# Kernel optimization log

Hardware: AMD Instinct MI355X
Metric: run time of the kernel (lower is better)

## Reference

```python
import jax, jax.numpy as jnp
import numpy as np

N_NODES = 100000
N_EDGES = 3200000
DROP_P = 0.5


def gcn_conv(x, W, b, src, dst, deg_inv_sqrt, n):
    # PyG GCNConv with self-loops already folded into (src, dst):
    # out[j] = sum_{(i->j)} dinv[i]*dinv[j] * (x W)[i] + b
    h = x @ W
    norm = deg_inv_sqrt[src] * deg_inv_sqrt[dst]          # [E+N]
    msg = h[src] * norm[:, None]                          # [E+N, d_out]
    out = jax.ops.segment_sum(msg, dst, num_segments=n)
    return out + b


def dropout(x, key, p=DROP_P):
    keep = jax.random.bernoulli(key, 1.0 - p, x.shape)
    return jnp.where(keep, x / (1.0 - p), 0.0)


def setup_inputs() -> dict:
    key = jax.random.key(0)
    ks = jax.random.split(key, 8)
    x = jax.random.normal(ks[0], (N_NODES, 64), dtype=jnp.float32)
    edge_index = jax.random.randint(ks[1], (2, N_EDGES), 0, N_NODES, dtype=jnp.int64)
    def glorot(k, fin, fout):
        lim = float(np.sqrt(6.0 / (fin + fout)))
        return jax.random.uniform(k, (fin, fout), jnp.float32, -lim, lim)
    return {
        "x": x,
        "edge_index": edge_index,
        "W1": glorot(ks[2], 64, 32), "b1": jnp.zeros((32,), jnp.float32),
        "W2": glorot(ks[3], 32, 64), "b2": jnp.zeros((64,), jnp.float32),
        "W3": glorot(ks[4], 64, 32), "b3": jnp.zeros((32,), jnp.float32),
    }


def reference(x, edge_index, W1, b1, W2, b2, W3, b3):
    n = x.shape[0]
    loops = jnp.arange(n, dtype=edge_index.dtype)
    src = jnp.concatenate([edge_index[0], loops])          # [E+N]
    dst = jnp.concatenate([edge_index[1], loops])
    deg = jax.ops.segment_sum(jnp.ones_like(dst, dtype=x.dtype), dst, num_segments=n)
    deg_inv_sqrt = jnp.where(deg > 0, jax.lax.rsqrt(deg), 0.0)

    dkey = jax.random.key(42)
    k1, k2 = jax.random.split(dkey)

    h = gcn_conv(x, W1, b1, src, dst, deg_inv_sqrt, n)
    h = jax.nn.celu(h)
    h = dropout(h, k1)
    h = gcn_conv(h, W2, b2, src, dst, deg_inv_sqrt, n)
    h = jax.nn.celu(h)
    h = dropout(h, k2)
    h = gcn_conv(h, W3, b3, src, dst, deg_inv_sqrt, n)
    return jax.nn.celu(h)
```

## Files before the change

kernel.cpp:

```cpp
#include <hip/hip_runtime.h>
#include <stdint.h>
#include <stddef.h>

typedef _Float16 half_t;
typedef _Float16 half4 __attribute__((ext_vector_type(4)));
typedef _Float16 half8 __attribute__((ext_vector_type(8)));

__host__ __device__ __forceinline__ uint32_t rotl32(uint32_t v, uint32_t r) {
  return (v << r) | (v >> (32u - r));
}

__host__ __device__ __forceinline__ void tf2x32(uint32_t k0, uint32_t k1,
                                                uint32_t x0, uint32_t x1,
                                                uint32_t& o0, uint32_t& o1) {
  uint32_t ks2 = k0 ^ k1 ^ 0x1BD11BDAu;
  x0 += k0; x1 += k1;
  x0 += x1; x1 = rotl32(x1, 13); x1 ^= x0;
  x0 += x1; x1 = rotl32(x1, 15); x1 ^= x0;
  x0 += x1; x1 = rotl32(x1, 26); x1 ^= x0;
  x0 += x1; x1 = rotl32(x1, 6);  x1 ^= x0;
  x0 += k1; x1 += ks2 + 1u;
  x0 += x1; x1 = rotl32(x1, 17); x1 ^= x0;
  x0 += x1; x1 = rotl32(x1, 29); x1 ^= x0;
  x0 += x1; x1 = rotl32(x1, 16); x1 ^= x0;
  x0 += x1; x1 = rotl32(x1, 24); x1 ^= x0;
  x0 += ks2; x1 += k0 + 2u;
  x0 += x1; x1 = rotl32(x1, 13); x1 ^= x0;
  x0 += x1; x1 = rotl32(x1, 15); x1 ^= x0;
  x0 += x1; x1 = rotl32(x1, 26); x1 ^= x0;
  x0 += x1; x1 = rotl32(x1, 6);  x1 ^= x0;
  x0 += k0; x1 += k1 + 3u;
  x0 += x1; x1 = rotl32(x1, 17); x1 ^= x0;
  x0 += x1; x1 = rotl32(x1, 29); x1 ^= x0;
  x0 += x1; x1 = rotl32(x1, 16); x1 ^= x0;
  x0 += x1; x1 = rotl32(x1, 24); x1 ^= x0;
  x0 += k1; x1 += ks2 + 4u;
  x0 += x1; x1 = rotl32(x1, 13); x1 ^= x0;
  x0 += x1; x1 = rotl32(x1, 15); x1 ^= x0;
  x0 += x1; x1 = rotl32(x1, 26); x1 ^= x0;
  x0 += x1; x1 = rotl32(x1, 6);  x1 ^= x0;
  x0 += ks2; x1 += k0 + 5u;
  o0 = x0; o1 = x1;
}

__device__ __forceinline__ bool tf_keep(uint32_t k0, uint32_t k1, uint32_t idx) {
  uint32_t o0, o1;
  tf2x32(k0, k1, 0u, idx, o0, o1);
  return ((o0 ^ o1) >> 31) == 0u;
}

#define CHUNK 4096
#define STASH 5120

__global__ __launch_bounds__(1024) void zero1024(uint32_t* __restrict__ p) {
  p[threadIdx.x] = 0u;
}

__global__ __launch_bounds__(256) void k4_binhist(const int* __restrict__ src,
                                                  const int* __restrict__ dst,
                                                  uint32_t* __restrict__ tbl,
                                                  uint32_t* __restrict__ gbcnt,
                                                  uint32_t* __restrict__ staging,
                                                  int E, int NB) {
  __shared__ uint32_t lcur[1024];
  __shared__ uint32_t ls[256];
  __shared__ uint32_t stage[CHUNK];
  int tid = threadIdx.x;
  for (int i = tid; i < NB; i += 256) lcur[i] = 0u;
  __syncthreads();
  int base = blockIdx.x * CHUNK;
  int end = min(base + CHUNK, E);
  uint32_t dv[16], sv[16];
  int m = 0;
  for (int i = base + tid; i < end; i += 256) {
    dv[m] = (uint32_t)dst[i];
    sv[m] = (uint32_t)src[i];
    ++m;
  }
  for (int q = 0; q < m; ++q) atomicAdd(&lcur[dv[q] >> 7], 1u);
  __syncthreads();
  uint32_t carry = 0u;
  for (int seg = 0; seg < 1024; seg += 256) {
    int i = seg + tid;
    uint32_t v = (i < NB) ? lcur[i] : 0u;
    ls[tid] = v;
    __syncthreads();
    for (int off = 1; off < 256; off <<= 1) {
      uint32_t t = (tid >= off) ? ls[tid - off] : 0u;
      __syncthreads();
      if (tid >= off) ls[tid] += t;
      __syncthreads();
    }
    uint32_t excl = carry + ls[tid] - v;
    if (i < NB) {
      tbl[(size_t)blockIdx.x * NB + i] = (excl << 16) | v;
      if (v) atomicAdd(&gbcnt[i], v);
      lcur[i] = excl;
    }
    carry += ls[255];
    __syncthreads();
  }
  for (int q = 0; q < m; ++q) {
    uint32_t d = dv[q];
    uint32_t p = atomicAdd(&lcur[d >> 7], 1u);
    stage[p] = ((d & 127u) << 17) | sv[q];
  }
  __syncthreads();
  int cnt_total = end - base;
  uint32_t* outp = staging + (size_t)blockIdx.x * CHUNK;
  for (int i = tid; i < cnt_total; i += 256) outp[i] = stage[i];
}

__global__ __launch_bounds__(1024) void k3_bscan(const uint32_t* __restrict__ gbcnt,
                                                 uint32_t* __restrict__ bbase, int NB) {
  __shared__ uint32_t s[1024];
  int i = threadIdx.x;
  uint32_t v = (i < NB) ? gbcnt[i] : 0u;
  s[i] = v;
  __syncthreads();
  for (int off = 1; off < 1024; off <<= 1) {
    uint32_t t = (i >= off) ? s[i - off] : 0u;
    __syncthreads();
    if (i >= off) s[i] += t;
    __syncthreads();
  }
  if (i < NB) bbase[i] = s[i] - v;
}

__global__ __launch_bounds__(1024) void k5_fin(
    const uint32_t* __restrict__ staging, const uint32_t* __restrict__ tbl,
    const uint32_t* __restrict__ bbase, uint32_t* __restrict__ rowp,
    float* __restrict__ dinv, uint32_t* __restrict__ esrc,
    int n, int E, int NBLK, int NB) {
  __shared__ uint32_t loff[1024];
  __shared__ uint32_t P[1025];
  __shared__ uint32_t ls[1024];
  __shared__ uint32_t stash[STASH];
  __shared__ uint32_t lc[128];
  __shared__ uint32_t sc[128];
  __shared__ uint32_t lcur[128];
  int tid = threadIdx.x;
  int b = blockIdx.x;
  if (tid < 128) lc[tid] = 0u;
  uint32_t packed = (tid < NBLK) ? tbl[(size_t)tid * NB + b] : 0u;
  uint32_t v = packed & 0xFFFFu;
  loff[tid] = packed >> 16;
  ls[tid] = v;
  __syncthreads();
  for (int off = 1; off < 1024; off <<= 1) {
    uint32_t t = (tid >= off) ? ls[tid - off] : 0u;
    __syncthreads();
    if (tid >= off) ls[tid] += t;
    __syncthreads();
  }
  P[tid] = ls[tid] - v;
  if (tid == 1023) P[1024] = ls[1023];
  __syncthreads();
  uint32_t total = P[NBLK];
  for (uint32_t q = (uint32_t)tid; q < total; q += 1024u) {
    int lo = 0, hi = NBLK;
    while (hi - lo > 1) {
      int mid = (lo + hi) >> 1;
      if (P[mid] <= q) lo = mid; else hi = mid;
    }
    uint32_t e = staging[(size_t)lo * CHUNK + loff[lo] + (q - P[lo])];
    if (q < (uint32_t)STASH) stash[q] = e;
    atomicAdd(&lc[e >> 17], 1u);
  }
  __syncthreads();
  uint32_t myc = (tid < 128) ? lc[tid] : 0u;
  if (tid < 128) sc[tid] = myc;
  __syncthreads();
  for (int off = 1; off < 128; off <<= 1) {
    uint32_t t = (tid < 128 && tid >= off) ? sc[tid - off] : 0u;
    __syncthreads();
    if (tid < 128 && tid >= off) sc[tid] += t;
    __syncthreads();
  }
  uint32_t s = bbase[b];
  if (tid < 128) {
    uint32_t gstart = s + sc[tid] - myc;
    int node = (b << 7) + tid;
    if (node < n) {
      rowp[node] = gstart;
      dinv[node] = 1.0f / sqrtf((float)(myc + 1u));
    }
    lcur[tid] = gstart;
  }
  if (b == 0 && tid == 0) rowp[n] = (uint32_t)E;
  __syncthreads();
  uint32_t lim = total < (uint32_t)STASH ? total : (uint32_t)STASH;
  for (uint32_t q = (uint32_t)tid; q < lim; q += 1024u) {
    uint32_t e = stash[q];
    uint32_t pos = atomicAdd(&lcur[e >> 17], 1u);
    esrc[pos] = e & 0x1FFFFu;
  }
  if (total > (uint32_t)STASH) {
    for (uint32_t q = (uint32_t)STASH + (uint32_t)tid; q < total; q += 1024u) {
      int lo = 0, hi = NBLK;
      while (hi - lo > 1) {
        int mid = (lo + hi) >> 1;
        if (P[mid] <= q) lo = mid; else hi = mid;
      }
      uint32_t e = staging[(size_t)lo * CHUNK + loff[lo] + (q - P[lo])];
      uint32_t pos = atomicAdd(&lcur[e >> 17], 1u);
      esrc[pos] = e & 0x1FFFFu;
    }
  }
}

__global__ __launch_bounds__(256) void gemm_n64_k32(
    const float* __restrict__ X, const float* __restrict__ W,
    const float* __restrict__ dinv, half_t* __restrict__ out16, int n) {
  __shared__ float Ws[64 * 32];
  __shared__ float Xs[32 * 68];
  int tid = threadIdx.x;
  {
    const float4* Wv = (const float4*)W;
    float4* Wsv = (float4*)Ws;
    Wsv[tid] = Wv[tid];
    Wsv[tid + 256] = Wv[tid + 256];
  }
  int row0 = blockIdx.x * 32;
  {
    const float4* Xv = (const float4*)(X + (size_t)row0 * 64);
    int lim = (n - row0) * 16;
    float4 z = make_float4(0.f, 0.f, 0.f, 0.f);
    int i0 = tid, i1 = tid + 256;
    float4 v0 = (i0 < lim) ? Xv[i0] : z;
    float4 v1 = (i1 < lim) ? Xv[i1] : z;
    *(float4*)(Xs + (i0 >> 4) * 68 + ((i0 & 15) << 2)) = v0;
    *(float4*)(Xs + (i1 >> 4) * 68 + ((i1 & 15) << 2)) = v1;
  }
  __syncthreads();
  int r = tid >> 3;
  int c4 = (tid & 7) << 2;
  int row = row0 + r;
  if (row >= n) return;
  float4 acc = make_float4(0.f, 0.f, 0.f, 0.f);
#pragma unroll
  for (int k = 0; k < 64; k += 4) {
    float4 xv = *(const float4*)(Xs + r * 68 + k);
    float4 w0 = *(const float4*)(Ws + (k + 0) * 32 + c4);
    float4 w1 = *(const float4*)(Ws + (k + 1) * 32 + c4);
    float4 w2 = *(const float4*)(Ws + (k + 2) * 32 + c4);
    float4 w3 = *(const float4*)(Ws + (k + 3) * 32 + c4);
    acc.x = fmaf(xv.x, w0.x, acc.x); acc.y = fmaf(xv.x, w0.y, acc.y);
    acc.z = fmaf(xv.x, w0.z, acc.z); acc.w = fmaf(xv.x, w0.w, acc.w);
    acc.x = fmaf(xv.y, w1.x, acc.x); acc.y = fmaf(xv.y, w1.y, acc.y);
    acc.z = fmaf(xv.y, w1.z, acc.z); acc.w = fmaf(xv.y, w1.w, acc.w);
    acc.x = fmaf(xv.z, w2.x, acc.x); acc.y = fmaf(xv.z, w2.y, acc.y);
    acc.z = fmaf(xv.z, w2.z, acc.z); acc.w = fmaf(xv.z, w2.w, acc.w);
    acc.x = fmaf(xv.w, w3.x, acc.x); acc.y = fmaf(xv.w, w3.y, acc.y);
    acc.z = fmaf(xv.w, w3.z, acc.z); acc.w = fmaf(xv.w, w3.w, acc.w);
  }
  float dj = dinv[row];
  half4 h;
  h.x = (half_t)(acc.x * dj); h.y = (half_t)(acc.y * dj);
  h.z = (half_t)(acc.z * dj); h.w = (half_t)(acc.w * dj);
  *(half4*)(out16 + (size_t)row * 32 + c4) = h;
}

__global__ __launch_bounds__(256) void gemm_k32_n64_act(
    const float* __restrict__ X, const float* __restrict__ W,
    const float* __restrict__ bias, float* __restrict__ out,
    uint32_t k0, uint32_t k1, int n) {
  __shared__ float Ws[32 * 64];
  __shared__ float Xs[16 * 36];
  int tid = threadIdx.x;
  {
    const float4* Wv = (const float4*)W;
    float4* Wsv = (float4*)Ws;
    Wsv[tid] = Wv[tid];
    Wsv[tid + 256] = Wv[tid + 256];
  }
  int row0 = blockIdx.x * 16;
  if (tid < 128) {
    const float4* Xv = (const float4*)(X + (size_t)row0 * 32);
    int lim = (n - row0) * 8;
    float4 z = make_float4(0.f, 0.f, 0.f, 0.f);
    float4 v = (tid < lim) ? Xv[tid] : z;
    *(float4*)(Xs + (tid >> 3) * 36 + ((tid & 7) << 2)) = v;
  }
  __syncthreads();
  int r = tid >> 4;
  int c4 = (tid & 15) << 2;
  int row = row0 + r;
  if (row >= n) return;
  float4 acc = make_float4(0.f, 0.f, 0.f, 0.f);
#pragma unroll
  for (int k = 0; k < 32; k += 4) {
    float4 xv = *(const float4*)(Xs + r * 36 + k);
    float4 w0 = *(const float4*)(Ws + (k + 0) * 64 + c4);
    float4 w1 = *(const float4*)(Ws + (k + 1) * 64 + c4);
    float4 w2 = *(const float4*)(Ws + (k + 2) * 64 + c4);
    float4 w3 = *(const float4*)(Ws + (k + 3) * 64 + c4);
    acc.x = fmaf(xv.x, w0.x, acc.x); acc.y = fmaf(xv.x, w0.y, acc.y);
    acc.z = fmaf(xv.x, w0.z, acc.z); acc.w = fmaf(xv.x, w0.w, acc.w);
    acc.x = fmaf(xv.y, w1.x, acc.x); acc.y = fmaf(xv.y, w1.y, acc.y);
    acc.z = fmaf(xv.y, w1.z, acc.z); acc.w = fmaf(xv.y, w1.w, acc.w);
    acc.x = fmaf(xv.z, w2.x, acc.x); acc.y = fmaf(xv.z, w2.y, acc.y);
    acc.z = fmaf(xv.z, w2.z, acc.z); acc.w = fmaf(xv.z, w2.w, acc.w);
    acc.x = fmaf(xv.w, w3.x, acc.x); acc.y = fmaf(xv.w, w3.y, acc.y);
    acc.z = fmaf(xv.w, w3.z, acc.z); acc.w = fmaf(xv.w, w3.w, acc.w);
  }
  float4 bv = *(const float4*)(bias + c4);
  float vv[4] = {acc.x + bv.x, acc.y + bv.y, acc.z + bv.z, acc.w + bv.w};
  uint32_t base = (uint32_t)row * 64u + (uint32_t)c4;
#pragma unroll
  for (int q = 0; q < 4; ++q) {
    float v = vv[q];
    v = v > 0.f ? v : expm1f(v);
    vv[q] = tf_keep(k0, k1, base + q) ? v * 2.f : 0.f;
  }
  *(float4*)(out + (size_t)row * 64 + c4) = make_float4(vv[0], vv[1], vv[2], vv[3]);
}

__global__ __launch_bounds__(256) void gather_fin(
    const half_t* __restrict__ hs, const uint32_t* __restrict__ rowp,
    const uint32_t* __restrict__ esrc, const float* __restrict__ dinv,
    const float* __restrict__ bias, float* __restrict__ outf,
    half_t* __restrict__ outh, int n, int mode, uint32_t k0, uint32_t k1,
    float fone) {
  __shared__ __align__(16) float ldsred[256];
  (void)fone;
  int tid = threadIdx.x;
  int gt = blockIdx.x * 256 + tid;
  int j = gt >> 5;
  int g = tid >> 5;
  int l = tid & 31;
  int eslot = l >> 2;
  int chunk = l & 3;
  float acc[8] = {0.f, 0.f, 0.f, 0.f, 0.f, 0.f, 0.f, 0.f};
  uint32_t e0 = 0, deg = 0;
  float selfv = 0.f, dj = 0.f;
  if (j < n) {
    e0 = rowp[j];
    deg = rowp[j + 1] - e0;
    selfv = (float)hs[(size_t)j * 32 + l];
    dj = dinv[j];
  }
  const half_t* hp = hs + (size_t)(chunk << 3);
  const half8 hz = {(half_t)0, (half_t)0, (half_t)0, (half_t)0,
                    (half_t)0, (half_t)0, (half_t)0, (half_t)0};
  for (uint32_t base = 0; base < deg; base += 32u) {
    uint32_t rem = deg - base;
    if (rem > 32u) rem = 32u;
    uint32_t li = (uint32_t)l < rem ? (uint32_t)l : rem - 1u;
    uint32_t idx = __builtin_nontemporal_load(&esrc[e0 + base + li]);
    half8 v0, v1, v2, v3;
#define GLOAD(KK, VOUT)                                                   \
    {                                                                     \
      uint32_t kp = ((uint32_t)(KK) << 3) + (uint32_t)eslot;              \
      uint32_t ks = kp < rem ? kp : rem - 1u;                             \
      uint32_t s = (uint32_t)__shfl((int)idx, (int)ks, 32);               \
      VOUT = hz;                                                          \
      if (kp < rem) VOUT = *(const half8*)(hp + ((size_t)s << 5));        \
    }
    GLOAD(0, v0)
    GLOAD(1, v1)
    GLOAD(2, v2)
    GLOAD(3, v3)
#undef GLOAD
    half8 s01 = v0 + v1;
    half8 s23 = v2 + v3;
#pragma unroll
    for (int q = 0; q < 8; ++q) {
      acc[q] += (float)s01[q];
      acc[q] += (float)s23[q];
    }
  }
#pragma unroll
  for (int m = 4; m <= 16; m <<= 1) {
#pragma unroll
    for (int q = 0; q < 8; ++q) acc[q] += __shfl_xor(acc[q], m);
  }
  if (l < 4) {
    *(float4*)(&ldsred[(g << 5) + (chunk << 3) + 0]) =
        make_float4(acc[0], acc[1], acc[2], acc[3]);
    *(float4*)(&ldsred[(g << 5) + (chunk << 3) + 4]) =
        make_float4(acc[4], acc[5], acc[6], acc[7]);
  }
  __builtin_amdgcn_wave_barrier();
  if (j >= n) return;
  float sum = ldsred[(g << 5) + l];
  sum += selfv;
  float v = dj * sum;
  if (mode == 1) {
    v += bias[l];
    v = v > 0.f ? v : expm1f(v);
    __builtin_nontemporal_store(v, &outf[gt]);
  } else if (mode == 3) {
    v += bias[l];
    v = v > 0.f ? v : expm1f(v);
    v = tf_keep(k0, k1, (uint32_t)gt) ? v * 2.f : 0.f;
    v *= dj;
    __builtin_nontemporal_store((half_t)v, &outh[gt]);
  } else {
    __builtin_nontemporal_store(v, &outf[gt]);
  }
}

extern "C" void kernel_launch(void* const* d_in, const int* in_sizes, int n_in,
                              void* d_out, int out_size, void* d_ws, size_t ws_size,
                              hipStream_t stream) {
  const float* x  = (const float*)d_in[0];
  const int*   ei = (const int*)d_in[1];
  const float* W1 = (const float*)d_in[2];
  const float* b1 = (const float*)d_in[3];
  const float* W2 = (const float*)d_in[4];
  const float* b2 = (const float*)d_in[5];
  const float* W3 = (const float*)d_in[6];
  const float* b3 = (const float*)d_in[7];
  float* out = (float*)d_out;

  const int n = in_sizes[0] / 64;
  const int E = in_sizes[1] / 2;
  const int* src = ei;
  const int* dst = ei + E;

  char* ws = (char*)d_ws;
  size_t off = 0;
  auto alloc = [&](size_t bytes) {
    void* p = ws + off;
    off = (off + bytes + 255) & ~(size_t)255;
    return p;
  };
  float*    A32   = (float*)alloc((size_t)n * 32 * 4);
  float*    C     = (float*)alloc((size_t)n * 64 * 4);
  half_t*   A16   = (half_t*)alloc((size_t)n * 32 * 2);
  half_t*   B16   = (half_t*)alloc((size_t)n * 32 * 2);
  float*    dinv  = (float*)alloc((size_t)n * 4);
  uint32_t* rowp  = (uint32_t*)alloc((size_t)(n + 1) * 4);
  uint32_t* esrc  = (uint32_t*)alloc((size_t)E * 4);
  uint32_t* gbcnt = (uint32_t*)alloc(1024 * 4);
  uint32_t* bbase = (uint32_t*)alloc(1024 * 4);
  uint32_t* staging = (uint32_t*)C;
  uint32_t* tbl     = (uint32_t*)A32;
  (void)ws_size; (void)n_in; (void)out_size;

  uint32_t k1a, k1b, k2a, k2b;
  tf2x32(0u, 42u, 0u, 0u, k1a, k1b);
  tf2x32(0u, 42u, 0u, 1u, k2a, k2b);

  const int NB   = (n + 127) >> 7;
  const int NBLK = (E + CHUNK - 1) / CHUNK;
  const int nv   = n * 32;
  const int gV   = (nv + 255) / 256;
  const int gG1  = (n + 31) / 32;
  const int gG2  = (n + 15) / 16;
  dim3 blk(256);

  zero1024<<<1, dim3(1024), 0, stream>>>(gbcnt);
  k4_binhist<<<NBLK, blk, 0, stream>>>(src, dst, tbl, gbcnt, staging, E, NB);
  k3_bscan<<<1, dim3(1024), 0, stream>>>(gbcnt, bbase, NB);
  k5_fin<<<NB, dim3(1024), 0, stream>>>(staging, tbl, bbase, rowp, dinv, esrc, n, E, NBLK, NB);

  gemm_n64_k32<<<gG1, blk, 0, stream>>>(x, W1, dinv, A16, n);
  gather_fin<<<gV, blk, 0, stream>>>(A16, rowp, esrc, dinv, b1, nullptr, B16, n, 3, k1a, k1b, 1.0f);

  gather_fin<<<gV, blk, 0, stream>>>(B16, rowp, esrc, dinv, nullptr, A32, nullptr, n, 0, 0u, 0u, 1.0f);
  gemm_k32_n64_act<<<gG2, blk, 0, stream>>>(A32, W2, b2, C, k2a, k2b, n);

  gemm_n64_k32<<<gG1, blk, 0, stream>>>(C, W3, dinv, A16, n);
  gather_fin<<<gV, blk, 0, stream>>>(A16, rowp, esrc, dinv, b3, out, nullptr, n, 1, 0u, 0u, 1.0f);
}
```

Before: 325.0 us.

## Split 32-wide fp16 features into two 16-column planes gathered in separate passes

The GEMM now writes its fp16 output as two column-half planes (n×16 each), and each aggregation is split into two gather16 launches, one per plane. Each pass works on a smaller feature array that fits better in cache during the random neighbor gathers. The cost is reading the CSR indices twice. The binning table is also transposed so the k5_fin reads per bin are contiguous rather than strided.

```diff
diff --git a/kernel.cpp b/kernel.cpp
--- a/kernel.cpp
+++ b/kernel.cpp
@@ -61,7 +61,7 @@
                                                   uint32_t* __restrict__ tbl,
                                                   uint32_t* __restrict__ gbcnt,
                                                   uint32_t* __restrict__ staging,
-                                                  int E, int NB) {
+                                                  int E, int NB, int NBLK) {
   __shared__ uint32_t lcur[1024];
   __shared__ uint32_t ls[256];
   __shared__ uint32_t stage[CHUNK];
@@ -93,7 +93,7 @@
     }
     uint32_t excl = carry + ls[tid] - v;
     if (i < NB) {
-      tbl[(size_t)blockIdx.x * NB + i] = (excl << 16) | v;
+      tbl[(size_t)i * NBLK + blockIdx.x] = (excl << 16) | v;
       if (v) atomicAdd(&gbcnt[i], v);
       lcur[i] = excl;
     }
@@ -142,7 +142,7 @@
   int tid = threadIdx.x;
   int b = blockIdx.x;
   if (tid < 128) lc[tid] = 0u;
-  uint32_t packed = (tid < NBLK) ? tbl[(size_t)tid * NB + b] : 0u;
+  uint32_t packed = (tid < NBLK) ? tbl[(size_t)b * NBLK + tid] : 0u;
   uint32_t v = packed & 0xFFFFu;
   loff[tid] = packed >> 16;
   ls[tid] = v;
@@ -258,7 +258,9 @@
   half4 h;
   h.x = (half_t)(acc.x * dj); h.y = (half_t)(acc.y * dj);
   h.z = (half_t)(acc.z * dj); h.w = (half_t)(acc.w * dj);
-  *(half4*)(out16 + (size_t)row * 32 + c4) = h;
+  int hf = c4 >> 4;
+  int cc = c4 & 15;
+  *(half4*)(out16 + (size_t)hf * ((size_t)n * 16) + (size_t)row * 16 + cc) = h;
 }
 
 __global__ __launch_bounds__(256) void gemm_k32_n64_act(
@@ -316,28 +318,26 @@
   *(float4*)(out + (size_t)row * 64 + c4) = make_float4(vv[0], vv[1], vv[2], vv[3]);
 }
 
-__global__ __launch_bounds__(256) void gather_fin(
+__global__ __launch_bounds__(256) void gather16(
     const half_t* __restrict__ hs, const uint32_t* __restrict__ rowp,
     const uint32_t* __restrict__ esrc, const float* __restrict__ dinv,
     const float* __restrict__ bias, float* __restrict__ outf,
     half_t* __restrict__ outh, int n, int mode, uint32_t k0, uint32_t k1,
-    float fone) {
+    uint32_t coff) {
   __shared__ __align__(16) float ldsred[256];
-  (void)fone;
   int tid = threadIdx.x;
-  int gt = blockIdx.x * 256 + tid;
-  int j = gt >> 5;
-  int g = tid >> 5;
-  int l = tid & 31;
-  int eslot = l >> 2;
-  int chunk = l & 3;
+  int g = tid >> 4;
+  int l = tid & 15;
+  int j = blockIdx.x * 16 + g;
+  int eslot = l >> 1;
+  int chunk = l & 1;
   float acc[8] = {0.f, 0.f, 0.f, 0.f, 0.f, 0.f, 0.f, 0.f};
   uint32_t e0 = 0, deg = 0;
   float selfv = 0.f, dj = 0.f;
   if (j < n) {
     e0 = rowp[j];
     deg = rowp[j + 1] - e0;
-    selfv = (float)hs[(size_t)j * 32 + l];
+    selfv = (float)hs[(size_t)j * 16 + l];
     dj = dinv[j];
   }
   const half_t* hp = hs + (size_t)(chunk << 3);
@@ -346,21 +346,23 @@
   for (uint32_t base = 0; base < deg; base += 32u) {
     uint32_t rem = deg - base;
     if (rem > 32u) rem = 32u;
-    uint32_t li = (uint32_t)l < rem ? (uint32_t)l : rem - 1u;
-    uint32_t idx = __builtin_nontemporal_load(&esrc[e0 + base + li]);
+    uint32_t li0 = (uint32_t)l < rem ? (uint32_t)l : rem - 1u;
+    uint32_t t1 = 16u + (uint32_t)l;
+    uint32_t li1 = t1 < rem ? t1 : rem - 1u;
+    uint32_t idx0 = __builtin_nontemporal_load(&esrc[e0 + base + li0]);
+    uint32_t idx1 = __builtin_nontemporal_load(&esrc[e0 + base + li1]);
     half8 v0, v1, v2, v3;
-#define GLOAD(KK, VOUT)                                                   \
+#define GLOAD(K, IDX, VOUT)                                               \
     {                                                                     \
-      uint32_t kp = ((uint32_t)(KK) << 3) + (uint32_t)eslot;              \
-      uint32_t ks = kp < rem ? kp : rem - 1u;                             \
-      uint32_t s = (uint32_t)__shfl((int)idx, (int)ks, 32);               \
+      uint32_t kp = (uint32_t)(K) + (uint32_t)eslot;                      \
+      uint32_t s = (uint32_t)__shfl((int)(IDX), (int)(kp & 15u), 16);     \
       VOUT = hz;                                                          \
-      if (kp < rem) VOUT = *(const half8*)(hp + ((size_t)s << 5));        \
-    }
-    GLOAD(0, v0)
-    GLOAD(1, v1)
-    GLOAD(2, v2)
-    GLOAD(3, v3)
+      if (kp < rem) VOUT = *(const half8*)(hp + ((size_t)s << 4));        \
+    }
+    GLOAD(0, idx0, v0)
+    GLOAD(8, idx0, v1)
+    GLOAD(16, idx1, v2)
+    GLOAD(24, idx1, v3)
 #undef GLOAD
     half8 s01 = v0 + v1;
     half8 s23 = v2 + v3;
@@ -371,33 +373,34 @@
     }
   }
 #pragma unroll
-  for (int m = 4; m <= 16; m <<= 1) {
+  for (int m = 2; m <= 8; m <<= 1) {
 #pragma unroll
     for (int q = 0; q < 8; ++q) acc[q] += __shfl_xor(acc[q], m);
   }
-  if (l < 4) {
-    *(float4*)(&ldsred[(g << 5) + (chunk << 3) + 0]) =
+  if (l < 2) {
+    *(float4*)(&ldsred[(g << 4) + (chunk << 3) + 0]) =
         make_float4(acc[0], acc[1], acc[2], acc[3]);
-    *(float4*)(&ldsred[(g << 5) + (chunk << 3) + 4]) =
+    *(float4*)(&ldsred[(g << 4) + (chunk << 3) + 4]) =
         make_float4(acc[4], acc[5], acc[6], acc[7]);
   }
   __builtin_amdgcn_wave_barrier();
   if (j >= n) return;
-  float sum = ldsred[(g << 5) + l];
+  float sum = ldsred[tid];
   sum += selfv;
   float v = dj * sum;
   if (mode == 1) {
     v += bias[l];
     v = v > 0.f ? v : expm1f(v);
-    __builtin_nontemporal_store(v, &outf[gt]);
+    __builtin_nontemporal_store(v, &outf[(size_t)j * 32 + l]);
   } else if (mode == 3) {
     v += bias[l];
     v = v > 0.f ? v : expm1f(v);
-    v = tf_keep(k0, k1, (uint32_t)gt) ? v * 2.f : 0.f;
+    uint32_t ridx = (uint32_t)j * 32u + coff + (uint32_t)l;
+    v = tf_keep(k0, k1, ridx) ? v * 2.f : 0.f;
     v *= dj;
-    __builtin_nontemporal_store((half_t)v, &outh[gt]);
+    __builtin_nontemporal_store((half_t)v, &outh[(size_t)j * 16 + l]);
   } else {
-    __builtin_nontemporal_store(v, &outf[gt]);
+    __builtin_nontemporal_store(v, &outf[(size_t)j * 32 + l]);
   }
 }
 
@@ -445,23 +448,26 @@
 
   const int NB   = (n + 127) >> 7;
   const int NBLK = (E + CHUNK - 1) / CHUNK;
-  const int nv   = n * 32;
-  const int gV   = (nv + 255) / 256;
+  const int gH   = (n + 15) / 16;
   const int gG1  = (n + 31) / 32;
   const int gG2  = (n + 15) / 16;
+  const size_t n16 = (size_t)n * 16;
   dim3 blk(256);
 
   zero1024<<<1, dim3(1024), 0, stream>>>(gbcnt);
-  k4_binhist<<<NBLK, blk, 0, stream>>>(src, dst, tbl, gbcnt, staging, E, NB);
+  k4_binhist<<<NBLK, blk, 0, stream>>>(src, dst, tbl, gbcnt, staging, E, NB, NBLK);
   k3_bscan<<<1, dim3(1024), 0, stream>>>(gbcnt, bbase, NB);
   k5_fin<<<NB, dim3(1024), 0, stream>>>(staging, tbl, bbase, rowp, dinv, esrc, n, E, NBLK, NB);
 
   gemm_n64_k32<<<gG1, blk, 0, stream>>>(x, W1, dinv, A16, n);
-  gather_fin<<<gV, blk, 0, stream>>>(A16, rowp, esrc, dinv, b1, nullptr, B16, n, 3, k1a, k1b, 1.0f);
-
-  gather_fin<<<gV, blk, 0, stream>>>(B16, rowp, esrc, dinv, nullptr, A32, nullptr, n, 0, 0u, 0u, 1.0f);
+  gather16<<<gH, blk, 0, stream>>>(A16,       rowp, esrc, dinv, b1,      nullptr,  B16,       n, 3, k1a, k1b, 0u);
+  gather16<<<gH, blk, 0, stream>>>(A16 + n16, rowp, esrc, dinv, b1 + 16, nullptr,  B16 + n16, n, 3, k1a, k1b, 16u);
+
+  gather16<<<gH, blk, 0, stream>>>(B16,       rowp, esrc, dinv, nullptr, A32,      nullptr,   n, 0, 0u, 0u, 0u);
+  gather16<<<gH, blk, 0, stream>>>(B16 + n16, rowp, esrc, dinv, nullptr, A32 + 16, nullptr,   n, 0, 0u, 0u, 16u);
   gemm_k32_n64_act<<<gG2, blk, 0, stream>>>(A32, W2, b2, C, k2a, k2b, n);
 
   gemm_n64_k32<<<gG1, blk, 0, stream>>>(C, W3, dinv, A16, n);
-  gather_fin<<<gV, blk, 0, stream>>>(A16, rowp, esrc, dinv, b3, out, nullptr, n, 1, 0u, 0u, 1.0f);
-}
+  gather16<<<gH, blk, 0, stream>>>(A16,       rowp, esrc, dinv, b3,      out,      nullptr,   n, 1, 0u, 0u, 0u);
+  gather16<<<gH, blk, 0, stream>>>(A16 + n16, rowp, esrc, dinv, b3 + 16, out + 16, nullptr,   n, 1, 0u, 0u, 16u);
+}
```

Result: slower. 378.7 us (+16.5%).
